# Performance work log

Measured on AMD Instinct MI355X. Metric: run time of the kernel, lower is better.

Reference implementation:

```python
import jax, jax.numpy as jnp
from jax import lax
import numpy as np

KK = 9  # 3x3 deformable kernel taps


def conv3x3(x, w, b):
    # x [N,C,H,W], w [O,I,3,3] (OIHW), stride 1, pad 1
    y = lax.conv_general_dilated(x, w, (1, 1), 'SAME',
                                 dimension_numbers=('NCHW', 'OIHW', 'NCHW'))
    return y + b[None, :, None, None]


def prelu(x, a):
    return jnp.where(x >= 0, x, a[None, :, None, None] * x)


def dcn(feat, offset, mask, w, b):
    # Modulated deformable conv (DCNv2), kernel 3x3, stride 1, pad 1, dg=1.
    # feat [N,C,H,W], offset [N,2*KK,H,W] (channel 2k = dy_k, 2k+1 = dx_k),
    # mask [N,KK,H,W], w [O,C,3,3].
    N, C, H, W = feat.shape
    O = w.shape[0]
    ky, kx = jnp.meshgrid(jnp.arange(3), jnp.arange(3), indexing='ij')
    ky = (ky - 1).reshape(KK).astype(feat.dtype)  # dilation 1, pad 1
    kx = (kx - 1).reshape(KK).astype(feat.dtype)
    off = offset.reshape(N, KK, 2, H, W)
    yy = jnp.arange(H, dtype=feat.dtype)[:, None]
    xx = jnp.arange(W, dtype=feat.dtype)[None, :]
    py = yy[None, None] + ky[None, :, None, None] + off[:, :, 0]  # [N,KK,H,W]
    px = xx[None, None] + kx[None, :, None, None] + off[:, :, 1]
    y0 = jnp.floor(py)
    x0 = jnp.floor(px)
    wy = py - y0
    wx = px - x0
    y0i = y0.astype(jnp.int32)
    x0i = x0.astype(jnp.int32)
    feat_flat = feat.reshape(N, C, H * W)

    def gather(yi, xi):
        valid = (yi >= 0) & (yi < H) & (xi >= 0) & (xi < W)
        yc = jnp.clip(yi, 0, H - 1)
        xc = jnp.clip(xi, 0, W - 1)
        idx = (yc * W + xc).reshape(N, 1, KK * H * W)
        g = jnp.take_along_axis(feat_flat, jnp.broadcast_to(idx, (N, C, KK * H * W)), axis=2)
        g = g.reshape(N, C, KK, H, W)
        return g * valid[:, None].astype(feat.dtype)

    v = (gather(y0i, x0i) * ((1 - wy) * (1 - wx))[:, None]
         + gather(y0i, x0i + 1) * ((1 - wy) * wx)[:, None]
         + gather(y0i + 1, x0i) * (wy * (1 - wx))[:, None]
         + gather(y0i + 1, x0i + 1) * (wy * wx)[:, None])  # [N,C,KK,H,W]
    v = v * mask[:, None]
    out = jnp.einsum('nckhw,ock->nohw', v, w.reshape(O, C, KK))
    return out + b[None, :, None, None]


def setup_inputs() -> dict:
    key = jax.random.key(0)
    ks = jax.random.split(key, 8)
    B, T, C, H, W = 8, 5, 3, 64, 64
    F = 64

    def winit(k, shape, fan_in, scale=1.0):
        return jax.random.normal(k, shape, jnp.float32) * (scale / np.sqrt(fan_in))

    return {
        'x': jax.random.normal(ks[0], (B, T, C, H, W), jnp.float32),
        'flow': jnp.zeros((T, B, 2, H, W), jnp.float32),  # unused (use_flow=False)
        'W_init': winit(ks[1], (F, C, 3, 3), C * 9),
        'b_init': jnp.zeros((F,), jnp.float32),
        'a_init': jnp.full((F,), 0.25, jnp.float32),
        'W_off': winit(ks[2], (F, 2 * C, 3, 3), 2 * C * 9),
        'b_off': jnp.zeros((F,), jnp.float32),
        'a_off': jnp.full((F,), 0.25, jnp.float32),
        'W_om': winit(ks[3], (3 * KK, F, 3, 3), F * 9, scale=0.1),  # small offsets
        'b_om': jnp.zeros((3 * KK,), jnp.float32),
        'W_dcn': winit(ks[4], (F, F, 3, 3), F * 9),
        'b_dcn': jnp.zeros((F,), jnp.float32),
    }


def reference(x, flow, W_init, b_init, a_init, W_off, b_off, a_off,
              W_om, b_om, W_dcn, b_dcn):
    B, T, C, H, W = x.shape
    xf = x.reshape(B * T, C, H, W)
    # per-frame feature extraction (batched over frames)
    feat = prelu(conv3x3(xf, W_init, b_init), a_init)             # [BT,F,H,W]
    # offset features from (reference frame 0, frame j) pairs
    ref0 = jnp.broadcast_to(x[:, :1], x.shape).reshape(B * T, C, H, W)
    pair = jnp.concatenate([ref0, xf], axis=1)                    # [BT,2C,H,W]
    off_feat = prelu(conv3x3(pair, W_off, b_off), a_off)          # [BT,F,H,W]
    # DCNv2 offset/mask head
    om = conv3x3(off_feat, W_om, b_om)                            # [BT,27,H,W]
    o1, o2, m = jnp.split(om, 3, axis=1)
    offset = jnp.concatenate([o1, o2], axis=1)                    # [BT,18,H,W]
    mask = jax.nn.sigmoid(m)                                      # [BT,9,H,W]
    out = dcn(feat, offset, mask, W_dcn, b_dcn)                   # [BT,F,H,W]
    return out.reshape(B, T, -1, H, W)
```

## Files before the change

### kernel.cpp

```cpp
#include <hip/hip_runtime.h>
#include <hip/hip_fp16.h>
#include <stdint.h>

typedef __attribute__((ext_vector_type(8))) _Float16 f16x8;
typedef __attribute__((ext_vector_type(4))) float f32x4;

#define NIMG 40
#define TFR  5
#define CIN  3
#define HH   64
#define WW   64
#define HW   4096
#define PPS  72
#define RSTR 72
#define CSTR 144

union U32H2 { uint u; __half2 h; };

__device__ __forceinline__ ushort4 f4_to_h4(f32x4 a) {
  ushort4 r;
  r.x = __half_as_ushort(__float2half(a[0]));
  r.y = __half_as_ushort(__float2half(a[1]));
  r.z = __half_as_ushort(__float2half(a[2]));
  r.w = __half_as_ushort(__float2half(a[3]));
  return r;
}
__device__ __forceinline__ void h4_add(f32x4& a, ushort4 s) {
  a[0] += __half2float(__ushort_as_half(s.x));
  a[1] += __half2float(__ushort_as_half(s.y));
  a[2] += __half2float(__ushort_as_half(s.z));
  a[3] += __half2float(__ushort_as_half(s.w));
}

__global__ __launch_bounds__(256) void k_wprep(
    const float* __restrict__ Wd, const float* __restrict__ Wom,
    const float* __restrict__ Wi, const float* __restrict__ Wo,
    __half* __restrict__ Waf, __half* __restrict__ Womf,
    __half* __restrict__ Wff, __half* __restrict__ Wof)
{
  int idx = blockIdx.x*256 + threadIdx.x;
  if (idx < 36864) {
    int j = idx & 7, lane = (idx >> 3) & 63;
    int grp = idx >> 9;
    int ot = grp & 3, tg = grp >> 2;
    int tap = tg % 9, kg = tg / 9;
    int row = lane & 15, ks = lane >> 4;
    int oc = ot*16 + row;
    int c  = kg*32 + ks*8 + j;
    Waf[idx] = __float2half(Wd[oc*576 + c*9 + tap]);
  } else if (idx < 36864 + 18432) {
    int q = idx - 36864;
    int j = q & 7, lane = (q >> 3) & 63;
    int grp = q >> 9;
    int k0 = grp % 18, mt = grp / 18;
    int row = lane & 15, ks = lane >> 4;
    int oc = mt*16 + row;
    int tap = k0 >> 1;
    int c = (k0 & 1)*32 + ks*8 + j;
    Womf[q] = (oc < 27) ? __float2half(Wom[oc*576 + c*9 + tap]) : __float2half(0.f);
  } else if (idx < 36864 + 18432 + 2048) {
    int q = idx - 36864 - 18432;
    int j = q & 7, lane = (q >> 3) & 63;
    int wv = q >> 9;
    int row = lane & 15, ks = lane >> 4;
    int f = wv*16 + row;
    int kk = ks*8 + j;
    Wff[q] = (kk < 27) ? __float2half(Wi[f*27 + kk]) : __float2half(0.f);
  } else if (idx < 36864 + 18432 + 2048 + 4096) {
    int q = idx - 36864 - 18432 - 2048;
    int j = q & 7, lane = (q >> 3) & 63;
    int grp = q >> 9;
    int wv = grp >> 1, half = grp & 1;
    int row = lane & 15, ks = lane >> 4;
    int f = wv*16 + row;
    int kk = half*32 + ks*8 + j;
    float v = 0.f;
    if (kk < 27)       v = Wo[f*54 + 27 + kk];
    else if (kk < 54)  v = Wo[f*54 + (kk - 27)];
    Wof[q] = __float2half(v);
  }
}

__global__ __launch_bounds__(256) void k_front(
    const float* __restrict__ x,
    const __half* __restrict__ Wff, const __half* __restrict__ Wof,
    const float* __restrict__ bi, const float* __restrict__ ai,
    const float* __restrict__ bo, const float* __restrict__ aof,
    __half* __restrict__ feat, __half* __restrict__ offf)
{
  __shared__ __align__(16) __half sp[32*PPS];
  int t = threadIdx.x, blk = blockIdx.x;
  int n = blk >> 7;
  int pbase = (blk & 127) * 32;
  int h = pbase >> 6;
  int wbase = pbase & 63;
  int n0 = (n/TFR)*TFR;
  const float* xc = x + (size_t)n*(CIN*HW);
  const float* xr = x + (size_t)n0*(CIN*HW);

  #pragma unroll
  for (int i = 0; i < 8; ++i) {
    int e = i*256 + t;
    int kk = e >> 5, px = e & 31;
    float v = 0.f;
    if (kk < 54) {
      int cur = (kk < 27);
      int kb = cur ? kk : kk - 27;
      int c = kb / 9, k = kb - c*9;
      int y  = h + k/3 - 1;
      int xx = wbase + px + (k - (k/3)*3) - 1;
      if (y >= 0 && y < HH && xx >= 0 && xx < WW)
        v = (cur ? xc : xr)[c*HW + y*WW + xx];
    }
    sp[px*PPS + kk] = __float2half(v);
  }
  __syncthreads();

  int wv = t >> 6, lane = t & 63;
  int row = lane & 15, ks = lane >> 4;
  f16x8 af0 = *(const f16x8*)(Wff + (wv<<9) + lane*8);
  f16x8 aw0 = *(const f16x8*)(Wof + (wv<<10) + lane*8);
  f16x8 aw1 = *(const f16x8*)(Wof + (wv<<10) + 512 + lane*8);
  #pragma unroll
  for (int nt = 0; nt < 2; ++nt) {
    const __half* bp = sp + (nt*16 + row)*PPS + ks*8;
    f16x8 b0 = *(const f16x8*)(bp);
    f16x8 b1 = *(const f16x8*)(bp + 32);
    f32x4 accf = {0.f,0.f,0.f,0.f}, acco = {0.f,0.f,0.f,0.f};
    accf = __builtin_amdgcn_mfma_f32_16x16x32_f16(af0, b0, accf, 0, 0, 0);
    acco = __builtin_amdgcn_mfma_f32_16x16x32_f16(aw0, b0, acco, 0, 0, 0);
    acco = __builtin_amdgcn_mfma_f32_16x16x32_f16(aw1, b1, acco, 0, 0, 0);
    int p  = pbase + nt*16 + row;
    int f0 = wv*16 + ks*4;
    size_t base = ((size_t)n*HW + p)*64 + f0;
    union { ushort4 u; __half b[4]; } pf, po;
    #pragma unroll
    for (int j = 0; j < 4; ++j) {
      float vf = accf[j] + bi[f0+j];
      float aF = ai[f0+j];
      vf = vf >= 0.f ? vf : aF*vf;
      pf.b[j] = __float2half(vf);
      float vo = acco[j] + bo[f0+j];
      float aO = aof[f0+j];
      vo = vo >= 0.f ? vo : aO*vo;
      po.b[j] = __float2half(vo);
    }
    *(ushort4*)(feat + base) = pf.u;
    *(ushort4*)(offf + base) = po.u;
  }
}

__global__ __launch_bounds__(256) void k_dcn(
    const __half* __restrict__ feat, const __half* __restrict__ offf,
    const __half* __restrict__ Waf, const __half* __restrict__ Womf,
    const float* __restrict__ bom, const float* __restrict__ bd,
    float* __restrict__ out)
{
  __shared__ __align__(16) char smem[5*36*CSTR];
  __shared__ __align__(16) char smem2[6912];
  __shared__ __half som[27*36];
  __shared__ int sflag;
  ushort4* soff = (ushort4*)smem2;
  uint4*   swgt = (uint4*)(smem2 + 2304);
  __half*  mbuf = (__half*)smem2;

  int t = threadIdx.x;
  int blk = blockIdx.x;
  int work = (blk & 7)*640 + (blk >> 3);
  int n = work >> 7;
  int pbase = (work & 127) * 32;
  int hrow = pbase >> 6, wbase = pbase & 63;
  int wv = t >> 6, lane = t & 63;
  int row = lane & 15, ks = lane >> 4;

  const char* ob = (const char*)(offf + (size_t)n*(HW*64));
  const char* fb = (const char*)(feat + (size_t)n*(HW*64));
  __half* region = (__half*)smem;
  char* sfeat = smem;

  if (t == 0) sflag = 1;

  uint4 wreg[6];
  #pragma unroll
  for (int i = 0; i < 6; ++i) {
    int u = i*256 + t;
    uint4 v = make_uint4(0,0,0,0);
    if (u < 1440) {
      int r = u / 288;
      int rem = u - r*288;
      int ci = rem >> 3, q = rem & 7;
      int y = hrow - 2 + r, xx = wbase - 2 + ci;
      if ((unsigned)y < 64u && (unsigned)xx < 64u)
        v = *(const uint4*)(fb + (((y<<6)+xx)<<7) + q*16);
    }
    wreg[i] = v;
  }

  for (int u = t; u < 816; u += 256) {
    int ry = u / 272;
    int rem = u - ry*272;
    int rx = rem >> 3, q = rem & 7;
    int y = hrow + ry - 1, xx = wbase + rx - 1;
    uint4 v = make_uint4(0,0,0,0);
    if ((unsigned)y < 64u && (unsigned)xx < 64u)
      v = *(const uint4*)(ob + (((y<<6)+xx)<<7) + q*16);
    *(uint4*)((char*)region + ((ry*34 + rx)*RSTR + q*8)*2) = v;
  }
  __syncthreads();

  {
    int mt = wv >> 1, nt = wv & 1;
    int pxl = nt*16 + row;
    f32x4 acc = {0.f,0.f,0.f,0.f};
    #pragma unroll
    for (int k0 = 0; k0 < 18; ++k0) {
      int k = k0 >> 1, ky = k/3, kx = k - ky*3;
      int c0 = (k0 & 1)*32;
      f16x8 a = *(const f16x8*)(Womf + ((mt*18 + k0)<<9) + lane*8);
      f16x8 b = *(const f16x8*)(region + (ky*34 + pxl + kx)*RSTR + c0 + ks*8);
      acc = __builtin_amdgcn_mfma_f32_16x16x32_f16(a, b, acc, 0, 0, 0);
    }
    #pragma unroll
    for (int j = 0; j < 4; ++j) {
      int oc = mt*16 + ks*4 + j;
      if (oc < 27) {
        float r = acc[j] + bom[oc];
        if (oc >= 18) r = 1.f/(1.f + __expf(-r));
        som[oc*36 + pxl] = __float2half(r);
      }
    }
  }
  __syncthreads();

  #pragma unroll
  for (int i = 0; i < 6; ++i) {
    int u = i*256 + t;
    if (u < 1440) {
      int r = u / 288;
      int rem = u - r*288;
      int ci = rem >> 3, q = rem & 7;
      *(uint4*)(sfeat + (r*36 + ci)*CSTR + q*16) = wreg[i];
    }
  }

  for (int e = t; e < 32*9; e += 256) {
    int px = e / 9, k = e - px*9;
    int w = wbase + px;
    float dy = __half2float(som[(2*k)*36 + px]);
    float dx = __half2float(som[(2*k+1)*36 + px]);
    float m  = __half2float(som[(18+k)*36 + px]);
    float py = (float)(hrow + (k/3) - 1) + dy;
    float qx = (float)(w + (k - (k/3)*3) - 1) + dx;
    float y0f = floorf(py), x0f = floorf(qx);
    float wy = py - y0f, wx = qx - x0f;
    int y0 = (int)y0f, x0 = (int)x0f;
    int y1 = y0 + 1, x1 = x0 + 1;
    float w00 = (1.f-wy)*(1.f-wx)*m;
    float w01 = (1.f-wy)*wx*m;
    float w10 = wy*(1.f-wx)*m;
    float w11 = wy*wx*m;
    if (y0 < 0 || y0 >= HH) { w00 = 0.f; w01 = 0.f; }
    if (y1 < 0 || y1 >= HH) { w10 = 0.f; w11 = 0.f; }
    if (x0 < 0 || x0 >= WW) { w00 = 0.f; w10 = 0.f; }
    if (x1 < 0 || x1 >= WW) { w01 = 0.f; w11 = 0.f; }
    int y0c = min(max(y0,0),HH-1), y1c = min(max(y1,0),HH-1);
    int x0c = min(max(x0,0),WW-1), x1c = min(max(x1,0),WW-1);
    int yw0 = y0c - (hrow-2), yw1 = y1c - (hrow-2);
    int xw0 = x0c - (wbase-2), xw1 = x1c - (wbase-2);
    bool ok = ((unsigned)yw0 < 5u) & ((unsigned)yw1 < 5u)
            & ((unsigned)xw0 < 36u) & ((unsigned)xw1 < 36u);
    if (!ok) atomicAnd(&sflag, 0);
    int cy0 = min(max(yw0,0),4), cy1 = min(max(yw1,0),4);
    int cx0 = min(max(xw0,0),35), cx1 = min(max(xw1,0),35);
    soff[e] = make_ushort4((ushort)((cy0*36 + cx0)*CSTR), (ushort)((cy0*36 + cx1)*CSTR),
                           (ushort)((cy1*36 + cx0)*CSTR), (ushort)((cy1*36 + cx1)*CSTR));
    U32H2 u00, u01, u10, u11;
    u00.h = __float2half2_rn(w00); u01.h = __float2half2_rn(w01);
    u10.h = __float2half2_rn(w10); u11.h = __float2half2_rn(w11);
    swgt[e] = make_uint4(u00.u, u01.u, u10.u, u11.u);
  }
  __syncthreads();

  int nt = wv & 1, kg = wv >> 1;
  int pxl = nt*16 + row;
  int cb = kg*64 + ks*16;
  f32x4 acc0 = {0.f,0.f,0.f,0.f}, acc1 = {0.f,0.f,0.f,0.f};
  f32x4 acc2 = {0.f,0.f,0.f,0.f}, acc3 = {0.f,0.f,0.f,0.f};
  const __half* afrag = Waf + (kg*9)*2048 + lane*8;

  if (sflag) {
    #pragma unroll
    for (int tap = 0; tap < 9; ++tap) {
      int e = pxl*9 + tap;
      ushort4 off = soff[e];
      uint4 wq  = swgt[e];
      U32H2 W00, W01, W10, W11;
      W00.u = wq.x; W01.u = wq.y; W10.u = wq.z; W11.u = wq.w;
      uint4 c00 = *(const uint4*)(sfeat + (int)off.x + cb);
      uint4 c01 = *(const uint4*)(sfeat + (int)off.y + cb);
      uint4 c10 = *(const uint4*)(sfeat + (int)off.z + cb);
      uint4 c11 = *(const uint4*)(sfeat + (int)off.w + cb);
      uint4 r;
#define BILIN(comp) { U32H2 a0v,a1v,a2v,a3v,res;                                \
      a0v.u = c00.comp; a1v.u = c01.comp; a2v.u = c10.comp; a3v.u = c11.comp;   \
      __half2 v = __hmul2(W00.h, a0v.h); v = __hfma2(W01.h, a1v.h, v);          \
      v = __hfma2(W10.h, a2v.h, v);      v = __hfma2(W11.h, a3v.h, v);          \
      res.h = v; r.comp = res.u; }
      BILIN(x) BILIN(y) BILIN(z) BILIN(w)
      f16x8 b = *(f16x8*)&r;
      const __half* ap = afrag + tap*2048;
      f16x8 a0 = *(const f16x8*)(ap);
      f16x8 a1 = *(const f16x8*)(ap + 512);
      f16x8 a2 = *(const f16x8*)(ap + 1024);
      f16x8 a3 = *(const f16x8*)(ap + 1536);
      acc0 = __builtin_amdgcn_mfma_f32_16x16x32_f16(a0, b, acc0, 0, 0, 0);
      acc1 = __builtin_amdgcn_mfma_f32_16x16x32_f16(a1, b, acc1, 0, 0, 0);
      acc2 = __builtin_amdgcn_mfma_f32_16x16x32_f16(a2, b, acc2, 0, 0, 0);
      acc3 = __builtin_amdgcn_mfma_f32_16x16x32_f16(a3, b, acc3, 0, 0, 0);
    }
  } else {
    #pragma unroll 1
    for (int tap = 0; tap < 9; ++tap) {
      float dy = __half2float(som[(2*tap)*36 + pxl]);
      float dx = __half2float(som[(2*tap+1)*36 + pxl]);
      float m  = __half2float(som[(18+tap)*36 + pxl]);
      int ky = tap/3, kx = tap - ky*3;
      float py = (float)(hrow + ky - 1) + dy;
      float qx = (float)(wbase + pxl + kx - 1) + dx;
      float y0f = floorf(py), x0f = floorf(qx);
      float wy = py - y0f, wx = qx - x0f;
      int y0 = (int)y0f, x0 = (int)x0f;
      int y1 = y0 + 1, x1 = x0 + 1;
      float w00 = (1.f-wy)*(1.f-wx)*m;
      float w01 = (1.f-wy)*wx*m;
      float w10 = wy*(1.f-wx)*m;
      float w11 = wy*wx*m;
      if (y0 < 0 || y0 >= HH) { w00 = 0.f; w01 = 0.f; }
      if (y1 < 0 || y1 >= HH) { w10 = 0.f; w11 = 0.f; }
      if (x0 < 0 || x0 >= WW) { w00 = 0.f; w10 = 0.f; }
      if (x1 < 0 || x1 >= WW) { w01 = 0.f; w11 = 0.f; }
      int y0c = min(max(y0,0),HH-1), y1c = min(max(y1,0),HH-1);
      int x0c = min(max(x0,0),WW-1), x1c = min(max(x1,0),WW-1);
      int o00 = (((y0c<<6)+x0c)<<7), o01 = (((y0c<<6)+x1c)<<7);
      int o10 = (((y1c<<6)+x0c)<<7), o11 = (((y1c<<6)+x1c)<<7);
      U32H2 W00, W01, W10, W11;
      W00.h = __float2half2_rn(w00); W01.h = __float2half2_rn(w01);
      W10.h = __float2half2_rn(w10); W11.h = __float2half2_rn(w11);
      uint4 c00 = *(const uint4*)(fb + o00 + cb);
      uint4 c01 = *(const uint4*)(fb + o01 + cb);
      uint4 c10 = *(const uint4*)(fb + o10 + cb);
      uint4 c11 = *(const uint4*)(fb + o11 + cb);
      uint4 r;
      BILIN(x) BILIN(y) BILIN(z) BILIN(w)
#undef BILIN
      f16x8 b = *(f16x8*)&r;
      const __half* ap = afrag + tap*2048;
      f16x8 a0 = *(const f16x8*)(ap);
      f16x8 a1 = *(const f16x8*)(ap + 512);
      f16x8 a2 = *(const f16x8*)(ap + 1024);
      f16x8 a3 = *(const f16x8*)(ap + 1536);
      acc0 = __builtin_amdgcn_mfma_f32_16x16x32_f16(a0, b, acc0, 0, 0, 0);
      acc1 = __builtin_amdgcn_mfma_f32_16x16x32_f16(a1, b, acc1, 0, 0, 0);
      acc2 = __builtin_amdgcn_mfma_f32_16x16x32_f16(a2, b, acc2, 0, 0, 0);
      acc3 = __builtin_amdgcn_mfma_f32_16x16x32_f16(a3, b, acc3, 0, 0, 0);
    }
  }
  __syncthreads();

  if (kg == 1) {
    int mb = pxl*72 + ks*4;
    *(ushort4*)(mbuf + mb)      = f4_to_h4(acc0);
    *(ushort4*)(mbuf + mb + 16) = f4_to_h4(acc1);
    *(ushort4*)(mbuf + mb + 32) = f4_to_h4(acc2);
    *(ushort4*)(mbuf + mb + 48) = f4_to_h4(acc3);
  }
  __syncthreads();
  if (kg == 0) {
    int mb = pxl*72 + ks*4;
    h4_add(acc0, *(ushort4*)(mbuf + mb));
    h4_add(acc1, *(ushort4*)(mbuf + mb + 16));
    h4_add(acc2, *(ushort4*)(mbuf + mb + 32));
    h4_add(acc3, *(ushort4*)(mbuf + mb + 48));
    int p = pbase + pxl;
    float* op = out + (size_t)n*(64*HW) + p;
    #pragma unroll
    for (int j = 0; j < 4; ++j) {
      int oc = ks*4 + j;
      op[(oc     )*HW] = acc0[j] + bd[oc];
      op[(oc + 16)*HW] = acc1[j] + bd[oc + 16];
      op[(oc + 32)*HW] = acc2[j] + bd[oc + 32];
      op[(oc + 48)*HW] = acc3[j] + bd[oc + 48];
    }
  }
}

extern "C" void kernel_launch(void* const* d_in, const int* in_sizes, int n_in,
                              void* d_out, int out_size, void* d_ws, size_t ws_size,
                              hipStream_t stream)
{
  const float* x   = (const float*)d_in[0];
  const float* Wi  = (const float*)d_in[2];
  const float* bi  = (const float*)d_in[3];
  const float* ai  = (const float*)d_in[4];
  const float* Wo  = (const float*)d_in[5];
  const float* bo  = (const float*)d_in[6];
  const float* aof = (const float*)d_in[7];
  const float* Wom = (const float*)d_in[8];
  const float* bom = (const float*)d_in[9];
  const float* Wd  = (const float*)d_in[10];
  const float* bd  = (const float*)d_in[11];
  float* out = (float*)d_out;

  __half* feat = (__half*)d_ws;
  __half* offf = feat + (size_t)NIMG*HW*64;
  __half* Waf  = offf + (size_t)NIMG*HW*64;
  __half* Womf = Waf + 36864;
  __half* Wff  = Womf + 18432;
  __half* Wof  = Wff + 2048;

  hipLaunchKernelGGL(k_wprep, dim3(240),         dim3(256), 0, stream,
                     Wd, Wom, Wi, Wo, Waf, Womf, Wff, Wof);
  hipLaunchKernelGGL(k_front, dim3(NIMG*HW/32),  dim3(256), 0, stream,
                     x, Wff, Wof, bi, ai, bo, aof, feat, offf);
  hipLaunchKernelGGL(k_dcn,   dim3(NIMG*HW/32),  dim3(256), 0, stream,
                     feat, offf, Waf, Womf, bom, bd, out);
}
```

Before: 87.09 us.

## Make DCN kernel persistent over five tiles with register-prefetched next-tile loads

The DCN kernel now launches 1024 blocks, and each block loops over five consecutive 32-pixel tiles instead of handling one. While the current tile is being computed, the offset-feature region and the feature window for the next tile are loaded from global memory into registers. This is meant to hide global load latency and spread block launch overhead across several tiles. In exchange it holds more registers per thread (launch bounds now request 4 blocks) and reduces the number of blocks that can overlap one another.

After: 287.4 us. +230.0%, slower.

```diff
diff --git a/kernel.cpp b/kernel.cpp
--- a/kernel.cpp
+++ b/kernel.cpp
@@ -150,7 +150,7 @@
   }
 }
 
-__global__ __launch_bounds__(256) void k_dcn(
+__global__ __launch_bounds__(256, 4) void k_dcn(
     const __half* __restrict__ feat, const __half* __restrict__ offf,
     const __half* __restrict__ Waf, const __half* __restrict__ Womf,
     const float* __restrict__ bom, const float* __restrict__ bd,
@@ -166,167 +166,127 @@
 
   int t = threadIdx.x;
   int blk = blockIdx.x;
-  int work = (blk & 7)*640 + (blk >> 3);
-  int n = work >> 7;
-  int pbase = (work & 127) * 32;
-  int hrow = pbase >> 6, wbase = pbase & 63;
+  int xcd = blk & 7, bidx = blk >> 3;
   int wv = t >> 6, lane = t & 63;
   int row = lane & 15, ks = lane >> 4;
-
-  const char* ob = (const char*)(offf + (size_t)n*(HW*64));
-  const char* fb = (const char*)(feat + (size_t)n*(HW*64));
-  __half* region = (__half*)smem;
-  char* sfeat = smem;
-
-  if (t == 0) sflag = 1;
-
-  uint4 wreg[6];
-  #pragma unroll
-  for (int i = 0; i < 6; ++i) {
-    int u = i*256 + t;
-    uint4 v = make_uint4(0,0,0,0);
-    if (u < 1440) {
-      int r = u / 288;
-      int rem = u - r*288;
-      int ci = rem >> 3, q = rem & 7;
-      int y = hrow - 2 + r, xx = wbase - 2 + ci;
-      if ((unsigned)y < 64u && (unsigned)xx < 64u)
-        v = *(const uint4*)(fb + (((y<<6)+xx)<<7) + q*16);
-    }
-    wreg[i] = v;
-  }
-
-  for (int u = t; u < 816; u += 256) {
-    int ry = u / 272;
-    int rem = u - ry*272;
-    int rx = rem >> 3, q = rem & 7;
-    int y = hrow + ry - 1, xx = wbase + rx - 1;
-    uint4 v = make_uint4(0,0,0,0);
-    if ((unsigned)y < 64u && (unsigned)xx < 64u)
-      v = *(const uint4*)(ob + (((y<<6)+xx)<<7) + q*16);
-    *(uint4*)((char*)region + ((ry*34 + rx)*RSTR + q*8)*2) = v;
-  }
-  __syncthreads();
-
-  {
-    int mt = wv >> 1, nt = wv & 1;
-    int pxl = nt*16 + row;
-    f32x4 acc = {0.f,0.f,0.f,0.f};
-    #pragma unroll
-    for (int k0 = 0; k0 < 18; ++k0) {
-      int k = k0 >> 1, ky = k/3, kx = k - ky*3;
-      int c0 = (k0 & 1)*32;
-      f16x8 a = *(const f16x8*)(Womf + ((mt*18 + k0)<<9) + lane*8);
-      f16x8 b = *(const f16x8*)(region + (ky*34 + pxl + kx)*RSTR + c0 + ks*8);
-      acc = __builtin_amdgcn_mfma_f32_16x16x32_f16(a, b, acc, 0, 0, 0);
-    }
-    #pragma unroll
-    for (int j = 0; j < 4; ++j) {
-      int oc = mt*16 + ks*4 + j;
-      if (oc < 27) {
-        float r = acc[j] + bom[oc];
-        if (oc >= 18) r = 1.f/(1.f + __expf(-r));
-        som[oc*36 + pxl] = __float2half(r);
-      }
-    }
-  }
-  __syncthreads();
-
-  #pragma unroll
-  for (int i = 0; i < 6; ++i) {
-    int u = i*256 + t;
-    if (u < 1440) {
-      int r = u / 288;
-      int rem = u - r*288;
-      int ci = rem >> 3, q = rem & 7;
-      *(uint4*)(sfeat + (r*36 + ci)*CSTR + q*16) = wreg[i];
-    }
-  }
-
-  for (int e = t; e < 32*9; e += 256) {
-    int px = e / 9, k = e - px*9;
-    int w = wbase + px;
-    float dy = __half2float(som[(2*k)*36 + px]);
-    float dx = __half2float(som[(2*k+1)*36 + px]);
-    float m  = __half2float(som[(18+k)*36 + px]);
-    float py = (float)(hrow + (k/3) - 1) + dy;
-    float qx = (float)(w + (k - (k/3)*3) - 1) + dx;
-    float y0f = floorf(py), x0f = floorf(qx);
-    float wy = py - y0f, wx = qx - x0f;
-    int y0 = (int)y0f, x0 = (int)x0f;
-    int y1 = y0 + 1, x1 = x0 + 1;
-    float w00 = (1.f-wy)*(1.f-wx)*m;
-    float w01 = (1.f-wy)*wx*m;
-    float w10 = wy*(1.f-wx)*m;
-    float w11 = wy*wx*m;
-    if (y0 < 0 || y0 >= HH) { w00 = 0.f; w01 = 0.f; }
-    if (y1 < 0 || y1 >= HH) { w10 = 0.f; w11 = 0.f; }
-    if (x0 < 0 || x0 >= WW) { w00 = 0.f; w10 = 0.f; }
-    if (x1 < 0 || x1 >= WW) { w01 = 0.f; w11 = 0.f; }
-    int y0c = min(max(y0,0),HH-1), y1c = min(max(y1,0),HH-1);
-    int x0c = min(max(x0,0),WW-1), x1c = min(max(x1,0),WW-1);
-    int yw0 = y0c - (hrow-2), yw1 = y1c - (hrow-2);
-    int xw0 = x0c - (wbase-2), xw1 = x1c - (wbase-2);
-    bool ok = ((unsigned)yw0 < 5u) & ((unsigned)yw1 < 5u)
-            & ((unsigned)xw0 < 36u) & ((unsigned)xw1 < 36u);
-    if (!ok) atomicAnd(&sflag, 0);
-    int cy0 = min(max(yw0,0),4), cy1 = min(max(yw1,0),4);
-    int cx0 = min(max(xw0,0),35), cx1 = min(max(xw1,0),35);
-    soff[e] = make_ushort4((ushort)((cy0*36 + cx0)*CSTR), (ushort)((cy0*36 + cx1)*CSTR),
-                           (ushort)((cy1*36 + cx0)*CSTR), (ushort)((cy1*36 + cx1)*CSTR));
-    U32H2 u00, u01, u10, u11;
-    u00.h = __float2half2_rn(w00); u01.h = __float2half2_rn(w01);
-    u10.h = __float2half2_rn(w10); u11.h = __float2half2_rn(w11);
-    swgt[e] = make_uint4(u00.u, u01.u, u10.u, u11.u);
-  }
-  __syncthreads();
-
   int nt = wv & 1, kg = wv >> 1;
   int pxl = nt*16 + row;
   int cb = kg*64 + ks*16;
-  f32x4 acc0 = {0.f,0.f,0.f,0.f}, acc1 = {0.f,0.f,0.f,0.f};
-  f32x4 acc2 = {0.f,0.f,0.f,0.f}, acc3 = {0.f,0.f,0.f,0.f};
   const __half* afrag = Waf + (kg*9)*2048 + lane*8;
-
-  if (sflag) {
+  __half* region = (__half*)smem;
+  char* sfeat = smem;
+
+  uint4 rreg[4], wreg[6];
+
+  auto region_issue = [&](int work_) {
+    int n_ = work_ >> 7;
+    int pb_ = (work_ & 127) * 32;
+    int hr_ = pb_ >> 6, wb_ = pb_ & 63;
+    const char* ob_ = (const char*)(offf + (size_t)n_*(HW*64));
     #pragma unroll
-    for (int tap = 0; tap < 9; ++tap) {
-      int e = pxl*9 + tap;
-      ushort4 off = soff[e];
-      uint4 wq  = swgt[e];
-      U32H2 W00, W01, W10, W11;
-      W00.u = wq.x; W01.u = wq.y; W10.u = wq.z; W11.u = wq.w;
-      uint4 c00 = *(const uint4*)(sfeat + (int)off.x + cb);
-      uint4 c01 = *(const uint4*)(sfeat + (int)off.y + cb);
-      uint4 c10 = *(const uint4*)(sfeat + (int)off.z + cb);
-      uint4 c11 = *(const uint4*)(sfeat + (int)off.w + cb);
-      uint4 r;
-#define BILIN(comp) { U32H2 a0v,a1v,a2v,a3v,res;                                \
-      a0v.u = c00.comp; a1v.u = c01.comp; a2v.u = c10.comp; a3v.u = c11.comp;   \
-      __half2 v = __hmul2(W00.h, a0v.h); v = __hfma2(W01.h, a1v.h, v);          \
-      v = __hfma2(W10.h, a2v.h, v);      v = __hfma2(W11.h, a3v.h, v);          \
-      res.h = v; r.comp = res.u; }
-      BILIN(x) BILIN(y) BILIN(z) BILIN(w)
-      f16x8 b = *(f16x8*)&r;
-      const __half* ap = afrag + tap*2048;
-      f16x8 a0 = *(const f16x8*)(ap);
-      f16x8 a1 = *(const f16x8*)(ap + 512);
-      f16x8 a2 = *(const f16x8*)(ap + 1024);
-      f16x8 a3 = *(const f16x8*)(ap + 1536);
-      acc0 = __builtin_amdgcn_mfma_f32_16x16x32_f16(a0, b, acc0, 0, 0, 0);
-      acc1 = __builtin_amdgcn_mfma_f32_16x16x32_f16(a1, b, acc1, 0, 0, 0);
-      acc2 = __builtin_amdgcn_mfma_f32_16x16x32_f16(a2, b, acc2, 0, 0, 0);
-      acc3 = __builtin_amdgcn_mfma_f32_16x16x32_f16(a3, b, acc3, 0, 0, 0);
-    }
-  } else {
-    #pragma unroll 1
-    for (int tap = 0; tap < 9; ++tap) {
-      float dy = __half2float(som[(2*tap)*36 + pxl]);
-      float dx = __half2float(som[(2*tap+1)*36 + pxl]);
-      float m  = __half2float(som[(18+tap)*36 + pxl]);
-      int ky = tap/3, kx = tap - ky*3;
-      float py = (float)(hrow + ky - 1) + dy;
-      float qx = (float)(wbase + pxl + kx - 1) + dx;
+    for (int i = 0; i < 4; ++i) {
+      int u = i*256 + t;
+      uint4 v = make_uint4(0,0,0,0);
+      if (u < 816) {
+        int ry = u / 272;
+        int rem = u - ry*272;
+        int rx = rem >> 3, q = rem & 7;
+        int y = hr_ + ry - 1, xx = wb_ + rx - 1;
+        if ((unsigned)y < 64u && (unsigned)xx < 64u)
+          v = *(const uint4*)(ob_ + (((y<<6)+xx)<<7) + q*16);
+      }
+      rreg[i] = v;
+    }
+  };
+  auto window_issue = [&](int work_) {
+    int n_ = work_ >> 7;
+    int pb_ = (work_ & 127) * 32;
+    int hr_ = pb_ >> 6, wb_ = pb_ & 63;
+    const char* fb_ = (const char*)(feat + (size_t)n_*(HW*64));
+    #pragma unroll
+    for (int i = 0; i < 6; ++i) {
+      int u = i*256 + t;
+      uint4 v = make_uint4(0,0,0,0);
+      if (u < 1440) {
+        int r = u / 288;
+        int rem = u - r*288;
+        int ci = rem >> 3, q = rem & 7;
+        int y = hr_ - 2 + r, xx = wb_ - 2 + ci;
+        if ((unsigned)y < 64u && (unsigned)xx < 64u)
+          v = *(const uint4*)(fb_ + (((y<<6)+xx)<<7) + q*16);
+      }
+      wreg[i] = v;
+    }
+  };
+
+  int work = xcd*640 + bidx*5;
+  region_issue(work);
+  window_issue(work);
+
+  for (int j = 0; j < 5; ++j, ++work) {
+    int n = work >> 7;
+    int pbase = (work & 127) * 32;
+    int hrow = pbase >> 6, wbase = pbase & 63;
+    const char* fb = (const char*)(feat + (size_t)n*(HW*64));
+
+    #pragma unroll
+    for (int i = 0; i < 4; ++i) {
+      int u = i*256 + t;
+      if (u < 816) {
+        int ry = u / 272;
+        int rem = u - ry*272;
+        int rx = rem >> 3, q = rem & 7;
+        *(uint4*)((char*)region + ((ry*34 + rx)*RSTR + q*8)*2) = rreg[i];
+      }
+    }
+    __syncthreads();
+
+    if (t == 0) sflag = 1;
+    if (j < 4) region_issue(work + 1);
+    {
+      int mt = wv >> 1, ntp = wv & 1;
+      int pxo = ntp*16 + row;
+      f32x4 acc = {0.f,0.f,0.f,0.f};
+      #pragma unroll
+      for (int k0 = 0; k0 < 18; ++k0) {
+        int k = k0 >> 1, ky = k/3, kx = k - ky*3;
+        int c0 = (k0 & 1)*32;
+        f16x8 a = *(const f16x8*)(Womf + ((mt*18 + k0)<<9) + lane*8);
+        f16x8 b = *(const f16x8*)(region + (ky*34 + pxo + kx)*RSTR + c0 + ks*8);
+        acc = __builtin_amdgcn_mfma_f32_16x16x32_f16(a, b, acc, 0, 0, 0);
+      }
+      #pragma unroll
+      for (int jj = 0; jj < 4; ++jj) {
+        int oc = mt*16 + ks*4 + jj;
+        if (oc < 27) {
+          float r = acc[jj] + bom[oc];
+          if (oc >= 18) r = 1.f/(1.f + __expf(-r));
+          som[oc*36 + pxo] = __float2half(r);
+        }
+      }
+    }
+    __syncthreads();
+
+    #pragma unroll
+    for (int i = 0; i < 6; ++i) {
+      int u = i*256 + t;
+      if (u < 1440) {
+        int r = u / 288;
+        int rem = u - r*288;
+        int ci = rem >> 3, q = rem & 7;
+        *(uint4*)(sfeat + (r*36 + ci)*CSTR + q*16) = wreg[i];
+      }
+    }
+    if (j < 4) window_issue(work + 1);
+
+    for (int e = t; e < 32*9; e += 256) {
+      int px = e / 9, k = e - px*9;
+      int w = wbase + px;
+      float dy = __half2float(som[(2*k)*36 + px]);
+      float dx = __half2float(som[(2*k+1)*36 + px]);
+      float m  = __half2float(som[(18+k)*36 + px]);
+      float py = (float)(hrow + (k/3) - 1) + dy;
+      float qx = (float)(w + (k - (k/3)*3) - 1) + dx;
       float y0f = floorf(py), x0f = floorf(qx);
       float wy = py - y0f, wx = qx - x0f;
       int y0 = (int)y0f, x0 = (int)x0f;
@@ -341,55 +301,127 @@
       if (x1 < 0 || x1 >= WW) { w01 = 0.f; w11 = 0.f; }
       int y0c = min(max(y0,0),HH-1), y1c = min(max(y1,0),HH-1);
       int x0c = min(max(x0,0),WW-1), x1c = min(max(x1,0),WW-1);
-      int o00 = (((y0c<<6)+x0c)<<7), o01 = (((y0c<<6)+x1c)<<7);
-      int o10 = (((y1c<<6)+x0c)<<7), o11 = (((y1c<<6)+x1c)<<7);
-      U32H2 W00, W01, W10, W11;
-      W00.h = __float2half2_rn(w00); W01.h = __float2half2_rn(w01);
-      W10.h = __float2half2_rn(w10); W11.h = __float2half2_rn(w11);
-      uint4 c00 = *(const uint4*)(fb + o00 + cb);
-      uint4 c01 = *(const uint4*)(fb + o01 + cb);
-      uint4 c10 = *(const uint4*)(fb + o10 + cb);
-      uint4 c11 = *(const uint4*)(fb + o11 + cb);
-      uint4 r;
-      BILIN(x) BILIN(y) BILIN(z) BILIN(w)
+      int yw0 = y0c - (hrow-2), yw1 = y1c - (hrow-2);
+      int xw0 = x0c - (wbase-2), xw1 = x1c - (wbase-2);
+      bool ok = ((unsigned)yw0 < 5u) & ((unsigned)yw1 < 5u)
+              & ((unsigned)xw0 < 36u) & ((unsigned)xw1 < 36u);
+      if (!ok) atomicAnd(&sflag, 0);
+      int cy0 = min(max(yw0,0),4), cy1 = min(max(yw1,0),4);
+      int cx0 = min(max(xw0,0),35), cx1 = min(max(xw1,0),35);
+      soff[e] = make_ushort4((ushort)((cy0*36 + cx0)*CSTR), (ushort)((cy0*36 + cx1)*CSTR),
+                             (ushort)((cy1*36 + cx0)*CSTR), (ushort)((cy1*36 + cx1)*CSTR));
+      U32H2 u00, u01, u10, u11;
+      u00.h = __float2half2_rn(w00); u01.h = __float2half2_rn(w01);
+      u10.h = __float2half2_rn(w10); u11.h = __float2half2_rn(w11);
+      swgt[e] = make_uint4(u00.u, u01.u, u10.u, u11.u);
+    }
+    __syncthreads();
+
+    f32x4 acc0 = {0.f,0.f,0.f,0.f}, acc1 = {0.f,0.f,0.f,0.f};
+    f32x4 acc2 = {0.f,0.f,0.f,0.f}, acc3 = {0.f,0.f,0.f,0.f};
+    if (sflag) {
+      #pragma unroll
+      for (int tap = 0; tap < 9; ++tap) {
+        int e = pxl*9 + tap;
+        ushort4 off = soff[e];
+        uint4 wq  = swgt[e];
+        U32H2 W00, W01, W10, W11;
+        W00.u = wq.x; W01.u = wq.y; W10.u = wq.z; W11.u = wq.w;
+        uint4 c00 = *(const uint4*)(sfeat + (int)off.x + cb);
+        uint4 c01 = *(const uint4*)(sfeat + (int)off.y + cb);
+        uint4 c10 = *(const uint4*)(sfeat + (int)off.z + cb);
+        uint4 c11 = *(const uint4*)(sfeat + (int)off.w + cb);
+        uint4 r;
+#define BILIN(comp) { U32H2 a0v,a1v,a2v,a3v,res;                                \
+        a0v.u = c00.comp; a1v.u = c01.comp; a2v.u = c10.comp; a3v.u = c11.comp; \
+        __half2 v = __hmul2(W00.h, a0v.h); v = __hfma2(W01.h, a1v.h, v);        \
+        v = __hfma2(W10.h, a2v.h, v);      v = __hfma2(W11.h, a3v.h, v);        \
+        res.h = v; r.comp = res.u; }
+        BILIN(x) BILIN(y) BILIN(z) BILIN(w)
+        f16x8 b = *(f16x8*)&r;
+        const __half* ap = afrag + tap*2048;
+        f16x8 a0 = *(const f16x8*)(ap);
+        f16x8 a1 = *(const f16x8*)(ap + 512);
+        f16x8 a2 = *(const f16x8*)(ap + 1024);
+        f16x8 a3 = *(const f16x8*)(ap + 1536);
+        acc0 = __builtin_amdgcn_mfma_f32_16x16x32_f16(a0, b, acc0, 0, 0, 0);
+        acc1 = __builtin_amdgcn_mfma_f32_16x16x32_f16(a1, b, acc1, 0, 0, 0);
+        acc2 = __builtin_amdgcn_mfma_f32_16x16x32_f16(a2, b, acc2, 0, 0, 0);
+        acc3 = __builtin_amdgcn_mfma_f32_16x16x32_f16(a3, b, acc3, 0, 0, 0);
+      }
+    } else {
+      #pragma unroll 1
+      for (int tap = 0; tap < 9; ++tap) {
+        float dy = __half2float(som[(2*tap)*36 + pxl]);
+        float dx = __half2float(som[(2*tap+1)*36 + pxl]);
+        float m  = __half2float(som[(18+tap)*36 + pxl]);
+        int ky = tap/3, kx = tap - ky*3;
+        float py = (float)(hrow + ky - 1) + dy;
+        float qx = (float)(wbase + pxl + kx - 1) + dx;
+        float y0f = floorf(py), x0f = floorf(qx);
+        float wy = py - y0f, wx = qx - x0f;
+        int y0 = (int)y0f, x0 = (int)x0f;
+        int y1 = y0 + 1, x1 = x0 + 1;
+        float w00 = (1.f-wy)*(1.f-wx)*m;
+        float w01 = (1.f-wy)*wx*m;
+        float w10 = wy*(1.f-wx)*m;
+        float w11 = wy*wx*m;
+        if (y0 < 0 || y0 >= HH) { w00 = 0.f; w01 = 0.f; }
+        if (y1 < 0 || y1 >= HH) { w10 = 0.f; w11 = 0.f; }
+        if (x0 < 0 || x0 >= WW) { w00 = 0.f; w10 = 0.f; }
+        if (x1 < 0 || x1 >= WW) { w01 = 0.f; w11 = 0.f; }
+        int y0c = min(max(y0,0),HH-1), y1c = min(max(y1,0),HH-1);
+        int x0c = min(max(x0,0),WW-1), x1c = min(max(x1,0),WW-1);
+        int o00 = (((y0c<<6)+x0c)<<7), o01 = (((y0c<<6)+x1c)<<7);
+        int o10 = (((y1c<<6)+x0c)<<7), o11 = (((y1c<<6)+x1c)<<7);
+        U32H2 W00, W01, W10, W11;
+        W00.h = __float2half2_rn(w00); W01.h = __float2half2_rn(w01);
+        W10.h = __float2half2_rn(w10); W11.h = __float2half2_rn(w11);
+        uint4 c00 = *(const uint4*)(fb + o00 + cb);
+        uint4 c01 = *(const uint4*)(fb + o01 + cb);
+        uint4 c10 = *(const uint4*)(fb + o10 + cb);
+        uint4 c11 = *(const uint4*)(fb + o11 + cb);
+        uint4 r;
+        BILIN(x) BILIN(y) BILIN(z) BILIN(w)
 #undef BILIN
-      f16x8 b = *(f16x8*)&r;
-      const __half* ap = afrag + tap*2048;
-      f16x8 a0 = *(const f16x8*)(ap);
-      f16x8 a1 = *(const f16x8*)(ap + 512);
-      f16x8 a2 = *(const f16x8*)(ap + 1024);
-      f16x8 a3 = *(const f16x8*)(ap + 1536);
-      acc0 = __builtin_amdgcn_mfma_f32_16x16x32_f16(a0, b, acc0, 0, 0, 0);
-      acc1 = __builtin_amdgcn_mfma_f32_16x16x32_f16(a1, b, acc1, 0, 0, 0);
-      acc2 = __builtin_amdgcn_mfma_f32_16x16x32_f16(a2, b, acc2, 0, 0, 0);
-      acc3 = __builtin_amdgcn_mfma_f32_16x16x32_f16(a3, b, acc3, 0, 0, 0);
-    }
-  }
-  __syncthreads();
-
-  if (kg == 1) {
-    int mb = pxl*72 + ks*4;
-    *(ushort4*)(mbuf + mb)      = f4_to_h4(acc0);
-    *(ushort4*)(mbuf + mb + 16) = f4_to_h4(acc1);
-    *(ushort4*)(mbuf + mb + 32) = f4_to_h4(acc2);
-    *(ushort4*)(mbuf + mb + 48) = f4_to_h4(acc3);
-  }
-  __syncthreads();
-  if (kg == 0) {
-    int mb = pxl*72 + ks*4;
-    h4_add(acc0, *(ushort4*)(mbuf + mb));
-    h4_add(acc1, *(ushort4*)(mbuf + mb + 16));
-    h4_add(acc2, *(ushort4*)(mbuf + mb + 32));
-    h4_add(acc3, *(ushort4*)(mbuf + mb + 48));
-    int p = pbase + pxl;
-    float* op = out + (size_t)n*(64*HW) + p;
-    #pragma unroll
-    for (int j = 0; j < 4; ++j) {
-      int oc = ks*4 + j;
-      op[(oc     )*HW] = acc0[j] + bd[oc];
-      op[(oc + 16)*HW] = acc1[j] + bd[oc + 16];
-      op[(oc + 32)*HW] = acc2[j] + bd[oc + 32];
-      op[(oc + 48)*HW] = acc3[j] + bd[oc + 48];
+        f16x8 b = *(f16x8*)&r;
+        const __half* ap = afrag + tap*2048;
+        f16x8 a0 = *(const f16x8*)(ap);
+        f16x8 a1 = *(const f16x8*)(ap + 512);
+        f16x8 a2 = *(const f16x8*)(ap + 1024);
+        f16x8 a3 = *(const f16x8*)(ap + 1536);
+        acc0 = __builtin_amdgcn_mfma_f32_16x16x32_f16(a0, b, acc0, 0, 0, 0);
+        acc1 = __builtin_amdgcn_mfma_f32_16x16x32_f16(a1, b, acc1, 0, 0, 0);
+        acc2 = __builtin_amdgcn_mfma_f32_16x16x32_f16(a2, b, acc2, 0, 0, 0);
+        acc3 = __builtin_amdgcn_mfma_f32_16x16x32_f16(a3, b, acc3, 0, 0, 0);
+      }
+    }
+    __syncthreads();
+
+    if (kg == 1) {
+      int mb = pxl*72 + ks*4;
+      *(ushort4*)(mbuf + mb)      = f4_to_h4(acc0);
+      *(ushort4*)(mbuf + mb + 16) = f4_to_h4(acc1);
+      *(ushort4*)(mbuf + mb + 32) = f4_to_h4(acc2);
+      *(ushort4*)(mbuf + mb + 48) = f4_to_h4(acc3);
+    }
+    __syncthreads();
+    if (kg == 0) {
+      int mb = pxl*72 + ks*4;
+      h4_add(acc0, *(ushort4*)(mbuf + mb));
+      h4_add(acc1, *(ushort4*)(mbuf + mb + 16));
+      h4_add(acc2, *(ushort4*)(mbuf + mb + 32));
+      h4_add(acc3, *(ushort4*)(mbuf + mb + 48));
+      int p = pbase + pxl;
+      float* op = out + (size_t)n*(64*HW) + p;
+      #pragma unroll
+      for (int jj = 0; jj < 4; ++jj) {
+        int oc = ks*4 + jj;
+        op[(oc     )*HW] = acc0[jj] + bd[oc];
+        op[(oc + 16)*HW] = acc1[jj] + bd[oc + 16];
+        op[(oc + 32)*HW] = acc2[jj] + bd[oc + 32];
+        op[(oc + 48)*HW] = acc3[jj] + bd[oc + 48];
+      }
     }
   }
 }
@@ -422,6 +454,6 @@
                      Wd, Wom, Wi, Wo, Waf, Womf, Wff, Wof);
   hipLaunchKernelGGL(k_front, dim3(NIMG*HW/32),  dim3(256), 0, stream,
                      x, Wff, Wof, bi, ai, bo, aof, feat, offf);
-  hipLaunchKernelGGL(k_dcn,   dim3(NIMG*HW/32),  dim3(256), 0, stream,
+  hipLaunchKernelGGL(k_dcn,   dim3(1024),        dim3(256), 0, stream,
                      feat, offf, Waf, Womf, bom, bd, out);
 }
```

## Split DCN output channels across twice as many waves per block

Applied to the files above, without the earlier changes.

Doubles the k_dcn block from 256 to 512 threads, adding an output-channel-half index so each wave computes two MFMA accumulators instead of four. The staging loads, the offset/mask head (now run only by half the waves) and the sampling-table build are redistributed over 512 threads. The goal is more latency hiding per block and fewer accumulator registers per thread (launch bounds 512,8). The cost is that each bilinear sample is now computed twice, once per channel half, and larger blocks may reduce scheduling flexibility.

New measurement: 96.41 us. 1.11x slower.

```diff
diff --git a/kernel.cpp b/kernel.cpp
--- a/kernel.cpp
+++ b/kernel.cpp
@@ -150,7 +150,7 @@
   }
 }
 
-__global__ __launch_bounds__(256) void k_dcn(
+__global__ __launch_bounds__(512, 8) void k_dcn(
     const __half* __restrict__ feat, const __half* __restrict__ offf,
     const __half* __restrict__ Waf, const __half* __restrict__ Womf,
     const float* __restrict__ bom, const float* __restrict__ bd,
@@ -172,6 +172,9 @@
   int hrow = pbase >> 6, wbase = pbase & 63;
   int wv = t >> 6, lane = t & 63;
   int row = lane & 15, ks = lane >> 4;
+  int nt = wv & 1, kg = (wv >> 1) & 1, oh = wv >> 2;
+  int pxl = nt*16 + row;
+  int cb = kg*64 + ks*16;
 
   const char* ob = (const char*)(offf + (size_t)n*(HW*64));
   const char* fb = (const char*)(feat + (size_t)n*(HW*64));
@@ -180,23 +183,30 @@
 
   if (t == 0) sflag = 1;
 
-  uint4 wreg[6];
-  #pragma unroll
-  for (int i = 0; i < 6; ++i) {
-    int u = i*256 + t;
-    uint4 v = make_uint4(0,0,0,0);
-    if (u < 1440) {
-      int r = u / 288;
-      int rem = u - r*288;
-      int ci = rem >> 3, q = rem & 7;
+  uint4 wreg0 = make_uint4(0,0,0,0), wreg1 = wreg0, wreg2 = wreg0;
+  {
+    int u0 = t, u1 = 512 + t, u2 = 1024 + t;
+    {
+      int r = u0 / 288, rem = u0 - r*288, ci = rem >> 3, q = rem & 7;
       int y = hrow - 2 + r, xx = wbase - 2 + ci;
       if ((unsigned)y < 64u && (unsigned)xx < 64u)
-        v = *(const uint4*)(fb + (((y<<6)+xx)<<7) + q*16);
-    }
-    wreg[i] = v;
-  }
-
-  for (int u = t; u < 816; u += 256) {
+        wreg0 = *(const uint4*)(fb + (((y<<6)+xx)<<7) + q*16);
+    }
+    {
+      int r = u1 / 288, rem = u1 - r*288, ci = rem >> 3, q = rem & 7;
+      int y = hrow - 2 + r, xx = wbase - 2 + ci;
+      if ((unsigned)y < 64u && (unsigned)xx < 64u)
+        wreg1 = *(const uint4*)(fb + (((y<<6)+xx)<<7) + q*16);
+    }
+    if (u2 < 1440) {
+      int r = u2 / 288, rem = u2 - r*288, ci = rem >> 3, q = rem & 7;
+      int y = hrow - 2 + r, xx = wbase - 2 + ci;
+      if ((unsigned)y < 64u && (unsigned)xx < 64u)
+        wreg2 = *(const uint4*)(fb + (((y<<6)+xx)<<7) + q*16);
+    }
+  }
+
+  for (int u = t; u < 816; u += 512) {
     int ry = u / 272;
     int rem = u - ry*272;
     int rx = rem >> 3, q = rem & 7;
@@ -208,9 +218,8 @@
   }
   __syncthreads();
 
-  {
-    int mt = wv >> 1, nt = wv & 1;
-    int pxl = nt*16 + row;
+  if (kg == 0) {
+    int mt = oh;
     f32x4 acc = {0.f,0.f,0.f,0.f};
     #pragma unroll
     for (int k0 = 0; k0 < 18; ++k0) {
@@ -232,18 +241,24 @@
   }
   __syncthreads();
 
-  #pragma unroll
-  for (int i = 0; i < 6; ++i) {
-    int u = i*256 + t;
-    if (u < 1440) {
-      int r = u / 288;
-      int rem = u - r*288;
-      int ci = rem >> 3, q = rem & 7;
-      *(uint4*)(sfeat + (r*36 + ci)*CSTR + q*16) = wreg[i];
-    }
-  }
-
-  for (int e = t; e < 32*9; e += 256) {
+  {
+    int u0 = t, u1 = 512 + t, u2 = 1024 + t;
+    {
+      int r = u0 / 288, rem = u0 - r*288, ci = rem >> 3, q = rem & 7;
+      *(uint4*)(sfeat + (r*36 + ci)*CSTR + q*16) = wreg0;
+    }
+    {
+      int r = u1 / 288, rem = u1 - r*288, ci = rem >> 3, q = rem & 7;
+      *(uint4*)(sfeat + (r*36 + ci)*CSTR + q*16) = wreg1;
+    }
+    if (u2 < 1440) {
+      int r = u2 / 288, rem = u2 - r*288, ci = rem >> 3, q = rem & 7;
+      *(uint4*)(sfeat + (r*36 + ci)*CSTR + q*16) = wreg2;
+    }
+  }
+
+  if (t < 288) {
+    int e = t;
     int px = e / 9, k = e - px*9;
     int w = wbase + px;
     float dy = __half2float(som[(2*k)*36 + px]);
@@ -281,12 +296,8 @@
   }
   __syncthreads();
 
-  int nt = wv & 1, kg = wv >> 1;
-  int pxl = nt*16 + row;
-  int cb = kg*64 + ks*16;
   f32x4 acc0 = {0.f,0.f,0.f,0.f}, acc1 = {0.f,0.f,0.f,0.f};
-  f32x4 acc2 = {0.f,0.f,0.f,0.f}, acc3 = {0.f,0.f,0.f,0.f};
-  const __half* afrag = Waf + (kg*9)*2048 + lane*8;
+  const __half* afrag = Waf + (kg*9)*2048 + (oh*2)*512 + lane*8;
 
   if (sflag) {
     #pragma unroll
@@ -311,12 +322,8 @@
       const __half* ap = afrag + tap*2048;
       f16x8 a0 = *(const f16x8*)(ap);
       f16x8 a1 = *(const f16x8*)(ap + 512);
-      f16x8 a2 = *(const f16x8*)(ap + 1024);
-      f16x8 a3 = *(const f16x8*)(ap + 1536);
       acc0 = __builtin_amdgcn_mfma_f32_16x16x32_f16(a0, b, acc0, 0, 0, 0);
       acc1 = __builtin_amdgcn_mfma_f32_16x16x32_f16(a1, b, acc1, 0, 0, 0);
-      acc2 = __builtin_amdgcn_mfma_f32_16x16x32_f16(a2, b, acc2, 0, 0, 0);
-      acc3 = __builtin_amdgcn_mfma_f32_16x16x32_f16(a3, b, acc3, 0, 0, 0);
     }
   } else {
     #pragma unroll 1
@@ -357,39 +364,29 @@
       const __half* ap = afrag + tap*2048;
       f16x8 a0 = *(const f16x8*)(ap);
       f16x8 a1 = *(const f16x8*)(ap + 512);
-      f16x8 a2 = *(const f16x8*)(ap + 1024);
-      f16x8 a3 = *(const f16x8*)(ap + 1536);
       acc0 = __builtin_amdgcn_mfma_f32_16x16x32_f16(a0, b, acc0, 0, 0, 0);
       acc1 = __builtin_amdgcn_mfma_f32_16x16x32_f16(a1, b, acc1, 0, 0, 0);
-      acc2 = __builtin_amdgcn_mfma_f32_16x16x32_f16(a2, b, acc2, 0, 0, 0);
-      acc3 = __builtin_amdgcn_mfma_f32_16x16x32_f16(a3, b, acc3, 0, 0, 0);
     }
   }
   __syncthreads();
 
   if (kg == 1) {
-    int mb = pxl*72 + ks*4;
+    int mb = pxl*72 + oh*32 + ks*4;
     *(ushort4*)(mbuf + mb)      = f4_to_h4(acc0);
     *(ushort4*)(mbuf + mb + 16) = f4_to_h4(acc1);
-    *(ushort4*)(mbuf + mb + 32) = f4_to_h4(acc2);
-    *(ushort4*)(mbuf + mb + 48) = f4_to_h4(acc3);
   }
   __syncthreads();
   if (kg == 0) {
-    int mb = pxl*72 + ks*4;
+    int mb = pxl*72 + oh*32 + ks*4;
     h4_add(acc0, *(ushort4*)(mbuf + mb));
     h4_add(acc1, *(ushort4*)(mbuf + mb + 16));
-    h4_add(acc2, *(ushort4*)(mbuf + mb + 32));
-    h4_add(acc3, *(ushort4*)(mbuf + mb + 48));
     int p = pbase + pxl;
     float* op = out + (size_t)n*(64*HW) + p;
     #pragma unroll
     for (int j = 0; j < 4; ++j) {
-      int oc = ks*4 + j;
+      int oc = oh*32 + ks*4 + j;
       op[(oc     )*HW] = acc0[j] + bd[oc];
       op[(oc + 16)*HW] = acc1[j] + bd[oc + 16];
-      op[(oc + 32)*HW] = acc2[j] + bd[oc + 32];
-      op[(oc + 48)*HW] = acc3[j] + bd[oc + 48];
     }
   }
 }
@@ -422,6 +419,6 @@
                      Wd, Wom, Wi, Wo, Waf, Womf, Wff, Wof);
   hipLaunchKernelGGL(k_front, dim3(NIMG*HW/32),  dim3(256), 0, stream,
                      x, Wff, Wof, bi, ai, bo, aof, feat, offf);
-  hipLaunchKernelGGL(k_dcn,   dim3(NIMG*HW/32),  dim3(256), 0, stream,
+  hipLaunchKernelGGL(k_dcn,   dim3(NIMG*HW/32),  dim3(512), 0, stream,
                      feat, offf, Waf, Womf, bom, bd, out);
 }
```
